# Optimization experiments

Hardware: AMD Instinct MI355X
Metric: run time of the kernel (lower is better)

## Reference

```python
import jax, jax.numpy as jnp
import numpy as np


def setup_inputs() -> dict:
    key = jax.random.key(0)
    k1, k2, k3, k4 = jax.random.split(key, 4)
    NUM_USERS, NUM_ITEMS, EMB_DIM, N_EDGES = 100000, 100000, 64, 1250000
    return {
        "u_emb": 0.1 * jax.random.normal(k1, (NUM_USERS, EMB_DIM), dtype=jnp.float32),
        "i_emb": 0.1 * jax.random.normal(k2, (NUM_ITEMS, EMB_DIM), dtype=jnp.float32),
        "u_idx": jax.random.randint(k3, (N_EDGES,), 0, NUM_USERS, dtype=jnp.int32),
        "i_idx": jax.random.randint(k4, (N_EDGES,), 0, NUM_ITEMS, dtype=jnp.int32),
    }


def reference(u_emb, i_emb, u_idx, i_idx):
    num_users = u_emb.shape[0]
    N = num_users + i_emb.shape[0]
    d = u_emb.shape[1]

    # global item indices; build symmetric directed edge list (2E messages)
    i_g = i_idx + num_users
    src = jnp.concatenate([u_idx, i_g])   # [2E]
    dst = jnp.concatenate([i_g, u_idx])   # [2E]

    # symmetric GCN normalization: w_e = deg(src)^-1/2 * deg(dst)^-1/2
    deg = jnp.zeros((N,), dtype=jnp.float32).at[src].add(1.0)
    d_inv_sqrt = jnp.where(deg > 0, jax.lax.rsqrt(jnp.maximum(deg, 1.0)), 0.0)
    w = d_inv_sqrt[src] * d_inv_sqrt[dst]  # [2E]

    def smooth(x):
        msgs = w[:, None] * x[src]          # [2E, d]
        return jnp.zeros((N, d), dtype=x.dtype).at[dst].add(msgs)

    x0 = jnp.concatenate([u_emb, i_emb], axis=0)  # [N, d]
    x1 = smooth(x0)
    x2 = smooth(x1)
    # embs_list = [x0, x1 + x0, x2 + x1]; mean over the 3 snapshots
    embs = (x0 + (x1 + x0) + (x2 + x1)) / 3.0
    return embs
```

## Files before the change

kernel.cpp:

```cpp
#include <hip/hip_runtime.h>

#define EMB_D 64
#define BN 64
#define LBITS 6
#define SRCBITS 18
#define SRCMASK ((1u << SRCBITS) - 1)
#define CURSTRIDE 16
#define BSCAN_T 256
#define BSCAN_I 16
#define CAPMAX 1280

typedef unsigned short u16;
typedef unsigned int u32;

__device__ __forceinline__ u16 f2bf(float f) {
    u32 u = __float_as_uint(f);
    return (u16)((u + 0x7FFFu + ((u >> 16) & 1u)) >> 16);
}
__device__ __forceinline__ float bf2f(u16 us) {
    return __uint_as_float((u32)us << 16);
}


__global__ void k_hist(const int* __restrict__ u_idx, const int* __restrict__ i_idx,
                       int* __restrict__ counts, int E, int num_users) {
    int e = blockIdx.x * blockDim.x + threadIdx.x;
    if (e < E) {
        int u = __builtin_nontemporal_load(u_idx + e);
        int iv = __builtin_nontemporal_load(i_idx + e);
        atomicAdd(&counts[u], 1);
        atomicAdd(&counts[num_users + iv], 1);
    }
}

__global__ void k_dis(const int* __restrict__ counts, float* __restrict__ dis, int N) {
    int n = blockIdx.x * blockDim.x + threadIdx.x;
    if (n < N) {
        int c = counts[n];
        dis[n] = c > 0 ? rsqrtf((float)c) : 0.0f;
    }
}


__global__ void k_bsize(const int* __restrict__ counts, int* __restrict__ bsize,
                        int N, int nbuckets) {
    int b = blockIdx.x * blockDim.x + threadIdx.x;
    if (b >= nbuckets) return;
    int lo = b << LBITS, hi = min(N, lo + BN);
    int s = 0;
    for (int n = lo; n < hi; n++) s += counts[n];
    bsize[b] = s;
}

__global__ void k_bscan(const int* __restrict__ bsize, int* __restrict__ boff,
                        int* __restrict__ cursors, int nb) {
    __shared__ int ssum[BSCAN_T];
    int t = threadIdx.x;
    int base = t * BSCAN_I;
    int v[BSCAN_I];
    int s = 0;
    for (int k = 0; k < BSCAN_I; k++) {
        int i = base + k;
        v[k] = (i < nb) ? bsize[i] : 0;
        s += v[k];
    }
    ssum[t] = s;
    __syncthreads();
    for (int off = 1; off < BSCAN_T; off <<= 1) {
        int tv = (t >= off) ? ssum[t - off] : 0;
        __syncthreads();
        ssum[t] += tv;
        __syncthreads();
    }
    int run = ssum[t] - s;
    for (int k = 0; k < BSCAN_I; k++) {
        int i = base + k;
        if (i < nb) {
            boff[i] = run;
            cursors[i * CURSTRIDE] = run;
        }
        run += v[k];
    }
    if (t == BSCAN_T - 1) boff[nb] = run;
}

__global__ void k_bucket_fill(const int* __restrict__ u_idx, const int* __restrict__ i_idx,
                              int* __restrict__ cursors, u32* __restrict__ entries,
                              int E, int num_users) {
    int e = blockIdx.x * blockDim.x + threadIdx.x;
    if (e >= E) return;
    int u  = __builtin_nontemporal_load(u_idx + e);
    int ig = num_users + __builtin_nontemporal_load(i_idx + e);
    int p = atomicAdd(&cursors[(u >> LBITS) * CURSTRIDE], 1);
    int q = atomicAdd(&cursors[(ig >> LBITS) * CURSTRIDE], 1);
    entries[p] = ((u32)(u & (BN - 1)) << SRCBITS) | (u32)ig;
    entries[q] = ((u32)(ig & (BN - 1)) << SRCBITS) | (u32)u;
}

__global__ __launch_bounds__(256) void k_bsort(u32* __restrict__ entries,
                                               const int* __restrict__ boff,
                                               int* __restrict__ B, int N) {
    __shared__ u32 se[CAPMAX];
    __shared__ int hcnt[BN];
    __shared__ int hcur[BN];
    int b = blockIdx.x, tid = threadIdx.x;
    int base = boff[b];
    int cnt = boff[b + 1] - base;
    if (cnt > CAPMAX) cnt = CAPMAX;
    for (int i = tid; i < cnt; i += 256) se[i] = entries[base + i];
    if (tid < BN) hcnt[tid] = 0;
    __syncthreads();
    for (int i = tid; i < cnt; i += 256) atomicAdd(&hcnt[se[i] >> SRCBITS], 1);
    __syncthreads();
    if (tid < 64) {
        int v = hcnt[tid];
        int inc = v;
        for (int d = 1; d < 64; d <<= 1) {
            int t = __shfl_up(inc, d);
            if (tid >= d) inc += t;
        }
        int excl = inc - v;
        hcur[tid] = excl;
        int n = (b << LBITS) + tid;
        if (n < N) B[n] = base + excl;
    }
    __syncthreads();
    for (int i = tid; i < cnt; i += 256) {
        u32 e = se[i];
        int dl = (int)(e >> SRCBITS);
        int pos = atomicAdd(&hcur[dl], 1);
        entries[base + pos] = e & SRCMASK;
    }
}

__global__ void k_prescale(const float* __restrict__ ue, const float* __restrict__ ie,
                           const float* __restrict__ dis, u16* __restrict__ xc,
                           int nuD, int totD) {
    int i4 = (blockIdx.x * blockDim.x + threadIdx.x) * 4;
    if (i4 >= totD) return;
    float d = dis[i4 >> 6];
    const float* src = (i4 < nuD) ? (ue + i4) : (ie + (i4 - nuD));
    float4 v = *(const float4*)src;
    u32 p01 = (u32)f2bf(d * v.x) | ((u32)f2bf(d * v.y) << 16);
    u32 p23 = (u32)f2bf(d * v.z) | ((u32)f2bf(d * v.w) << 16);
    *(uint2*)(xc + i4) = make_uint2(p01, p23);
}


__global__ void k_smooth1(const int* __restrict__ B, const int* __restrict__ counts,
                          const u32* __restrict__ adj,
                          const float* __restrict__ dis, const u16* __restrict__ xc0,
                          u16* __restrict__ xc1, int N) {
    int n = blockIdx.x * (blockDim.x >> 6) + (threadIdx.x >> 6);
    int lane = threadIdx.x & 63;
    if (n >= N) return;
    int start = B[n];
    int end = start + counts[n];
    float a0 = 0.f, a1 = 0.f, a2 = 0.f, a3 = 0.f;
    for (int base = start; base < end; base += 64) {
        int cnt = min(64, end - base);
        int nid = 0;
        if (lane < cnt) nid = (int)adj[base + lane];
        int j = 0;
        for (; j + 3 < cnt; j += 4) {
            int n0 = __shfl(nid, j),     n1 = __shfl(nid, j + 1);
            int n2 = __shfl(nid, j + 2), n3 = __shfl(nid, j + 3);
            a0 += bf2f(xc0[((size_t)n0 << 6) + lane]);
            a1 += bf2f(xc0[((size_t)n1 << 6) + lane]);
            a2 += bf2f(xc0[((size_t)n2 << 6) + lane]);
            a3 += bf2f(xc0[((size_t)n3 << 6) + lane]);
        }
        for (; j < cnt; j++) {
            int nj = __shfl(nid, j);
            a0 += bf2f(xc0[((size_t)nj << 6) + lane]);
        }
    }
    float d = dis[n];
    xc1[((size_t)n << 6) + lane] = f2bf(d * d * ((a0 + a1) + (a2 + a3)));
}

__global__ void k_smooth2(const int* __restrict__ B, const int* __restrict__ counts,
                          const u32* __restrict__ adj,
                          const float* __restrict__ dis,
                          const float* __restrict__ u_emb, const float* __restrict__ i_emb,
                          const u16* __restrict__ xc1, float* __restrict__ out,
                          int N, int num_users) {
    int n = blockIdx.x * (blockDim.x >> 6) + (threadIdx.x >> 6);
    int lane = threadIdx.x & 63;
    if (n >= N) return;
    int start = B[n];
    int deg = counts[n];
    int end = start + deg;
    float a0 = 0.f, a1 = 0.f, a2 = 0.f, a3 = 0.f;
    for (int base = start; base < end; base += 64) {
        int cnt = min(64, end - base);
        int nid = 0;
        if (lane < cnt) nid = (int)adj[base + lane];
        int j = 0;
        for (; j + 3 < cnt; j += 4) {
            int n0 = __shfl(nid, j),     n1 = __shfl(nid, j + 1);
            int n2 = __shfl(nid, j + 2), n3 = __shfl(nid, j + 3);
            a0 += bf2f(xc1[((size_t)n0 << 6) + lane]);
            a1 += bf2f(xc1[((size_t)n1 << 6) + lane]);
            a2 += bf2f(xc1[((size_t)n2 << 6) + lane]);
            a3 += bf2f(xc1[((size_t)n3 << 6) + lane]);
        }
        for (; j < cnt; j++) {
            int nj = __shfl(nid, j);
            a0 += bf2f(xc1[((size_t)nj << 6) + lane]);
        }
    }
    size_t o = ((size_t)n << 6) + lane;
    float x0v = (n < num_users) ? u_emb[o] : i_emb[o - (((size_t)num_users) << 6)];
    float x1v = bf2f(xc1[o]) * sqrtf((float)deg);
    out[o] = (2.0f * x0v + 2.0f * x1v + dis[n] * ((a0 + a1) + (a2 + a3))) * (1.0f / 3.0f);
}


extern "C" void kernel_launch(void* const* d_in, const int* in_sizes, int n_in,
                              void* d_out, int out_size, void* d_ws, size_t ws_size,
                              hipStream_t stream) {
    const float* u_emb = (const float*)d_in[0];
    const float* i_emb = (const float*)d_in[1];
    const int*   u_idx = (const int*)d_in[2];
    const int*   i_idx = (const int*)d_in[3];
    float* out = (float*)d_out;

    const int num_users = in_sizes[0] / EMB_D;
    const int num_items = in_sizes[1] / EMB_D;
    const int E = in_sizes[2];
    const int N = num_users + num_items;
    const int adjE = 2 * E;
    const int totD = N * EMB_D;
    const int nuD = num_users * EMB_D;
    const int nbuckets = (N + BN - 1) >> LBITS;

    auto align_up = [](size_t x) { return (x + 255) & ~(size_t)255; };
    char* p = (char*)d_ws;
    int*   counts  = (int*)p; p += align_up((size_t)N * 4);
    float* dis     = (float*)p; p += align_up((size_t)N * 4);
    int*   B       = (int*)p; p += align_up((size_t)N * 4);
    int*   bsize   = (int*)p; p += align_up((size_t)nbuckets * 4);
    int*   boff    = (int*)p; p += align_up((size_t)(nbuckets + 1) * 4);
    int*   cursors = (int*)p; p += align_up((size_t)nbuckets * CURSTRIDE * 4);
    u32*   entries = (u32*)p; p += align_up((size_t)adjE * 4);
    u16*   xc0     = (u16*)p; p += align_up((size_t)totD * 2);
    u16*   xc1     = (u16*)p;

    hipMemsetAsync(counts, 0, (size_t)N * 4, stream);

    const int blk = 256;
    k_hist<<<(E + blk - 1) / blk, blk, 0, stream>>>(u_idx, i_idx, counts, E, num_users);
    k_dis<<<(N + blk - 1) / blk, blk, 0, stream>>>(counts, dis, N);
    k_bsize<<<(nbuckets + blk - 1) / blk, blk, 0, stream>>>(counts, bsize, N, nbuckets);
    k_bscan<<<1, BSCAN_T, 0, stream>>>(bsize, boff, cursors, nbuckets);
    k_bucket_fill<<<(E + blk - 1) / blk, blk, 0, stream>>>(u_idx, i_idx, cursors, entries,
                                                           E, num_users);
    k_bsort<<<nbuckets, blk, 0, stream>>>(entries, boff, B, N);
    k_prescale<<<(totD / 4 + blk - 1) / blk, blk, 0, stream>>>(u_emb, i_emb, dis, xc0,
                                                               nuD, totD);
    int nodes_per_blk = blk / 64;
    int ggrid = (N + nodes_per_blk - 1) / nodes_per_blk;
    k_smooth1<<<ggrid, blk, 0, stream>>>(B, counts, entries, dis, xc0, xc1, N);
    k_smooth2<<<ggrid, blk, 0, stream>>>(B, counts, entries, dis, u_emb, i_emb, xc1, out,
                                         N, num_users);
}
```

Baseline: 542.6 us.

## Partition bucket fill by XCD so each die owns a bucket range

Replaces the per-edge bucket fill with a persistent kernel. Each block reads its XCC_ID and only inserts edges whose destination bucket falls in that die's bucket range. Blocks pull edge chunks from a per-XCD atomic work counter. The aim is to keep cursor atomics and entry writes local to one die's L2 and avoid cross-die coherence traffic, at the cost of every XCD reading the full edge list. Correctness assumes all 8 XCDs get at least one block, since a die with no blocks would leave its buckets unfilled.

```diff
diff --git a/kernel.cpp b/kernel.cpp
--- a/kernel.cpp
+++ b/kernel.cpp
@@ -9,6 +9,8 @@
 #define BSCAN_T 256
 #define BSCAN_I 16
 #define CAPMAX 1280
+#define NXCD 8
+#define CHUNK_IT 8
 
 typedef unsigned short u16;
 typedef unsigned int u32;
@@ -84,17 +86,41 @@
     if (t == BSCAN_T - 1) boff[nb] = run;
 }
 
-__global__ void k_bucket_fill(const int* __restrict__ u_idx, const int* __restrict__ i_idx,
-                              int* __restrict__ cursors, u32* __restrict__ entries,
-                              int E, int num_users) {
-    int e = blockIdx.x * blockDim.x + threadIdx.x;
-    if (e >= E) return;
-    int u  = __builtin_nontemporal_load(u_idx + e);
-    int ig = num_users + __builtin_nontemporal_load(i_idx + e);
-    int p = atomicAdd(&cursors[(u >> LBITS) * CURSTRIDE], 1);
-    int q = atomicAdd(&cursors[(ig >> LBITS) * CURSTRIDE], 1);
-    entries[p] = ((u32)(u & (BN - 1)) << SRCBITS) | (u32)ig;
-    entries[q] = ((u32)(ig & (BN - 1)) << SRCBITS) | (u32)u;
+__global__ void k_fill_xcd(const int* __restrict__ u_idx, const int* __restrict__ i_idx,
+                           int* __restrict__ cursors, u32* __restrict__ entries,
+                           int* __restrict__ chunk_cur, int E, int num_users,
+                           int bucket_range) {
+    u32 xcd;
+    asm("s_getreg_b32 %0, hwreg(HW_REG_XCC_ID)" : "=s"(xcd));
+    xcd &= (NXCD - 1);
+    const int blo = (int)xcd * bucket_range;
+    const int bhi = blo + bucket_range;
+    __shared__ int sbase;
+    const int chunk = 256 * CHUNK_IT;
+    for (;;) {
+        __syncthreads();
+        if (threadIdx.x == 0) sbase = atomicAdd(&chunk_cur[(int)xcd * CURSTRIDE], chunk);
+        __syncthreads();
+        int base = sbase;
+        if (base >= E) break;
+        #pragma unroll
+        for (int k = 0; k < CHUNK_IT; k++) {
+            int e = base + k * 256 + threadIdx.x;
+            if (e < E) {
+                int u  = __builtin_nontemporal_load(u_idx + e);
+                int ig = num_users + __builtin_nontemporal_load(i_idx + e);
+                int bu = u >> LBITS, bi = ig >> LBITS;
+                if (bu >= blo && bu < bhi) {
+                    int p = atomicAdd(&cursors[bu * CURSTRIDE], 1);
+                    entries[p] = ((u32)(u & (BN - 1)) << SRCBITS) | (u32)ig;
+                }
+                if (bi >= blo && bi < bhi) {
+                    int q = atomicAdd(&cursors[bi * CURSTRIDE], 1);
+                    entries[q] = ((u32)(ig & (BN - 1)) << SRCBITS) | (u32)u;
+                }
+            }
+        }
+    }
 }
 
 __global__ __launch_bounds__(256) void k_bsort(u32* __restrict__ entries,
@@ -234,28 +260,31 @@
     const int totD = N * EMB_D;
     const int nuD = num_users * EMB_D;
     const int nbuckets = (N + BN - 1) >> LBITS;
+    const int bucket_range = (nbuckets + NXCD - 1) / NXCD;
 
     auto align_up = [](size_t x) { return (x + 255) & ~(size_t)255; };
     char* p = (char*)d_ws;
-    int*   counts  = (int*)p; p += align_up((size_t)N * 4);
-    float* dis     = (float*)p; p += align_up((size_t)N * 4);
-    int*   B       = (int*)p; p += align_up((size_t)N * 4);
-    int*   bsize   = (int*)p; p += align_up((size_t)nbuckets * 4);
-    int*   boff    = (int*)p; p += align_up((size_t)(nbuckets + 1) * 4);
-    int*   cursors = (int*)p; p += align_up((size_t)nbuckets * CURSTRIDE * 4);
-    u32*   entries = (u32*)p; p += align_up((size_t)adjE * 4);
-    u16*   xc0     = (u16*)p; p += align_up((size_t)totD * 2);
-    u16*   xc1     = (u16*)p;
-
-    hipMemsetAsync(counts, 0, (size_t)N * 4, stream);
+    int*   counts    = (int*)p; p += align_up((size_t)N * 4);
+    int*   chunk_cur = (int*)p; p += align_up((size_t)NXCD * CURSTRIDE * 4);
+    float* dis       = (float*)p; p += align_up((size_t)N * 4);
+    int*   B         = (int*)p; p += align_up((size_t)N * 4);
+    int*   bsize     = (int*)p; p += align_up((size_t)nbuckets * 4);
+    int*   boff      = (int*)p; p += align_up((size_t)(nbuckets + 1) * 4);
+    int*   cursors   = (int*)p; p += align_up((size_t)nbuckets * CURSTRIDE * 4);
+    u32*   entries   = (u32*)p; p += align_up((size_t)adjE * 4);
+    u16*   xc0       = (u16*)p; p += align_up((size_t)totD * 2);
+    u16*   xc1      = (u16*)p;
+
+    hipMemsetAsync(counts, 0, align_up((size_t)N * 4) + align_up((size_t)NXCD * CURSTRIDE * 4),
+                   stream);
 
     const int blk = 256;
     k_hist<<<(E + blk - 1) / blk, blk, 0, stream>>>(u_idx, i_idx, counts, E, num_users);
     k_dis<<<(N + blk - 1) / blk, blk, 0, stream>>>(counts, dis, N);
     k_bsize<<<(nbuckets + blk - 1) / blk, blk, 0, stream>>>(counts, bsize, N, nbuckets);
     k_bscan<<<1, BSCAN_T, 0, stream>>>(bsize, boff, cursors, nbuckets);
-    k_bucket_fill<<<(E + blk - 1) / blk, blk, 0, stream>>>(u_idx, i_idx, cursors, entries,
-                                                           E, num_users);
+    k_fill_xcd<<<512, blk, 0, stream>>>(u_idx, i_idx, cursors, entries, chunk_cur,
+                                        E, num_users, bucket_range);
     k_bsort<<<nbuckets, blk, 0, stream>>>(entries, boff, B, N);
     k_prescale<<<(totD / 4 + blk - 1) / blk, blk, 0, stream>>>(u_emb, i_emb, dis, xc0,
                                                                nuD, totD);
```

After: 540.7 us. No clear change (-0.3%).

## Replace atomic bucket scatter with two-pass LDS-staged radix partition

Applied to the files above, without the earlier changes.

Replaces the per-edge global atomic bucket fill with a two-level radix partition. The first pass groups edges into 4096-node coarse buckets using a shared-memory histogram and one global atomic per bucket per block. The second pass splits each coarse bucket into 64-node buckets the same way. The bsort kernel now stages its sorted output in LDS and writes it back coalesced. The goal is to cut global atomic contention and scattered 4-byte writes, at the cost of an extra recA buffer, an extra full read/write pass over the edges, and more kernel launches.

```diff
diff --git a/kernel.cpp b/kernel.cpp
--- a/kernel.cpp
+++ b/kernel.cpp
@@ -3,12 +3,17 @@
 #define EMB_D 64
 #define BN 64
 #define LBITS 6
+#define CBN 4096
+#define CBBITS 12
 #define SRCBITS 18
 #define SRCMASK ((1u << SRCBITS) - 1)
 #define CURSTRIDE 16
 #define BSCAN_T 256
 #define BSCAN_I 16
 #define CAPMAX 1280
+#define P1_EDGES 1024
+#define P2_RECS 2048
+#define P2_CHUNKS 32
 
 typedef unsigned short u16;
 typedef unsigned int u32;
@@ -84,23 +89,137 @@
     if (t == BSCAN_T - 1) boff[nb] = run;
 }
 
-__global__ void k_bucket_fill(const int* __restrict__ u_idx, const int* __restrict__ i_idx,
-                              int* __restrict__ cursors, u32* __restrict__ entries,
-                              int E, int num_users) {
-    int e = blockIdx.x * blockDim.x + threadIdx.x;
-    if (e >= E) return;
-    int u  = __builtin_nontemporal_load(u_idx + e);
-    int ig = num_users + __builtin_nontemporal_load(i_idx + e);
-    int p = atomicAdd(&cursors[(u >> LBITS) * CURSTRIDE], 1);
-    int q = atomicAdd(&cursors[(ig >> LBITS) * CURSTRIDE], 1);
-    entries[p] = ((u32)(u & (BN - 1)) << SRCBITS) | (u32)ig;
-    entries[q] = ((u32)(ig & (BN - 1)) << SRCBITS) | (u32)u;
+__global__ void k_c1init(const int* __restrict__ boff, int* __restrict__ cursors1,
+                         int nCB, int nbuckets) {
+    int t = threadIdx.x;
+    if (t < nCB) cursors1[t * CURSTRIDE] = boff[min(t * (CBN / BN), nbuckets)];
+}
+
+__global__ __launch_bounds__(256) void k_part1(const int* __restrict__ u_idx,
+                                               const int* __restrict__ i_idx,
+                                               int* __restrict__ cursors1,
+                                               u32* __restrict__ recA,
+                                               int E, int num_users, int nCB) {
+    __shared__ u32 buf[2 * P1_EDGES];
+    __shared__ u16 slotcb[2 * P1_EDGES];
+    __shared__ int hist[64], lofs[64], gbase[64], lcur[64];
+    const int tid = threadIdx.x;
+    const int base = blockIdx.x * P1_EDGES;
+
+    if (tid < 64) hist[tid] = 0;
+    __syncthreads();
+
+    bool val[4]; int ru[4], rig[4];
+    #pragma unroll
+    for (int k = 0; k < 4; k++) {
+        int e = base + k * 256 + tid;
+        val[k] = e < E;
+        ru[k] = 0; rig[k] = 0;
+        if (val[k]) {
+            ru[k]  = __builtin_nontemporal_load(u_idx + e);
+            rig[k] = num_users + __builtin_nontemporal_load(i_idx + e);
+        }
+    }
+    #pragma unroll
+    for (int k = 0; k < 4; k++) if (val[k]) {
+        atomicAdd(&hist[rig[k] >> CBBITS], 1);
+        atomicAdd(&hist[ru[k] >> CBBITS], 1);
+    }
+    __syncthreads();
+    if (tid < 64) {
+        int v = hist[tid], inc = v;
+        for (int d = 1; d < 64; d <<= 1) {
+            int t2 = __shfl_up(inc, d);
+            if ((tid & 63) >= d) inc += t2;
+        }
+        lofs[tid] = inc - v;
+        lcur[tid] = inc - v;
+        gbase[tid] = (tid < nCB) ? atomicAdd(&cursors1[tid * CURSTRIDE], v) : 0;
+    }
+    __syncthreads();
+    #pragma unroll
+    for (int k = 0; k < 4; k++) if (val[k]) {
+        int u = ru[k], ig = rig[k];
+        int cb0 = ig >> CBBITS;
+        int p0 = atomicAdd(&lcur[cb0], 1);
+        buf[p0] = ((u32)(ig & (CBN - 1)) << SRCBITS) | (u32)u;
+        slotcb[p0] = (u16)cb0;
+        int cb1 = u >> CBBITS;
+        int p1 = atomicAdd(&lcur[cb1], 1);
+        buf[p1] = ((u32)(u & (CBN - 1)) << SRCBITS) | (u32)ig;
+        slotcb[p1] = (u16)cb1;
+    }
+    __syncthreads();
+    int tot = 2 * max(0, min(E - base, P1_EDGES));
+    for (int i = tid; i < tot; i += 256) {
+        int cb = slotcb[i];
+        recA[gbase[cb] + (i - lofs[cb])] = buf[i];
+    }
+}
+
+__global__ __launch_bounds__(256) void k_part2(const u32* __restrict__ recA,
+                                               u32* __restrict__ entries,
+                                               int* __restrict__ cursors2,
+                                               const int* __restrict__ boff,
+                                               int nbuckets) {
+    const int b = blockIdx.x / P2_CHUNKS;
+    const int c = blockIdx.x % P2_CHUNKS;
+    const int cbStart = boff[min(b * (CBN / BN), nbuckets)];
+    const int cbEnd   = boff[min((b + 1) * (CBN / BN), nbuckets)];
+    const int start = cbStart + c * P2_RECS;
+    if (start >= cbEnd) return;
+    const int cnt = min(P2_RECS, cbEnd - start);
+
+    __shared__ u32 buf[P2_RECS];
+    __shared__ u16 slotbin[P2_RECS];
+    __shared__ int hist[64], lofs[64], gbase[64], lcur[64];
+    const int tid = threadIdx.x;
+
+    if (tid < 64) hist[tid] = 0;
+    __syncthreads();
+
+    bool rv[8]; u32 rr[8];
+    #pragma unroll
+    for (int k = 0; k < 8; k++) {
+        int i = k * 256 + tid;
+        rv[k] = i < cnt;
+        rr[k] = rv[k] ? recA[start + i] : 0;
+    }
+    #pragma unroll
+    for (int k = 0; k < 8; k++) if (rv[k])
+        atomicAdd(&hist[(rr[k] >> (SRCBITS + LBITS)) & 63], 1);
+    __syncthreads();
+    if (tid < 64) {
+        int v = hist[tid], inc = v;
+        for (int d = 1; d < 64; d <<= 1) {
+            int t2 = __shfl_up(inc, d);
+            if ((tid & 63) >= d) inc += t2;
+        }
+        lofs[tid] = inc - v;
+        lcur[tid] = inc - v;
+        int gb = b * (CBN / BN) + tid;
+        gbase[tid] = (gb < nbuckets) ? atomicAdd(&cursors2[gb * CURSTRIDE], v) : 0;
+    }
+    __syncthreads();
+    #pragma unroll
+    for (int k = 0; k < 8; k++) if (rv[k]) {
+        int bin = (int)((rr[k] >> (SRCBITS + LBITS)) & 63);
+        int pos = atomicAdd(&lcur[bin], 1);
+        buf[pos] = rr[k];
+        slotbin[pos] = (u16)bin;
+    }
+    __syncthreads();
+    for (int i = tid; i < cnt; i += 256) {
+        int bin = slotbin[i];
+        entries[gbase[bin] + (i - lofs[bin])] = buf[i];
+    }
 }
 
 __global__ __launch_bounds__(256) void k_bsort(u32* __restrict__ entries,
                                                const int* __restrict__ boff,
                                                int* __restrict__ B, int N) {
     __shared__ u32 se[CAPMAX];
+    __shared__ u32 se2[CAPMAX];
     __shared__ int hcnt[BN];
     __shared__ int hcur[BN];
     int b = blockIdx.x, tid = threadIdx.x;
@@ -110,7 +229,7 @@
     for (int i = tid; i < cnt; i += 256) se[i] = entries[base + i];
     if (tid < BN) hcnt[tid] = 0;
     __syncthreads();
-    for (int i = tid; i < cnt; i += 256) atomicAdd(&hcnt[se[i] >> SRCBITS], 1);
+    for (int i = tid; i < cnt; i += 256) atomicAdd(&hcnt[(se[i] >> SRCBITS) & 63], 1);
     __syncthreads();
     if (tid < 64) {
         int v = hcnt[tid];
@@ -127,10 +246,12 @@
     __syncthreads();
     for (int i = tid; i < cnt; i += 256) {
         u32 e = se[i];
-        int dl = (int)(e >> SRCBITS);
+        int dl = (int)((e >> SRCBITS) & 63);
         int pos = atomicAdd(&hcur[dl], 1);
-        entries[base + pos] = e & SRCMASK;
-    }
+        se2[pos] = e & SRCMASK;
+    }
+    __syncthreads();
+    for (int i = tid; i < cnt; i += 256) entries[base + i] = se2[i];
 }
 
 __global__ void k_prescale(const float* __restrict__ ue, const float* __restrict__ ie,
@@ -234,18 +355,21 @@
     const int totD = N * EMB_D;
     const int nuD = num_users * EMB_D;
     const int nbuckets = (N + BN - 1) >> LBITS;
+    const int nCB = (N + CBN - 1) >> CBBITS;
 
     auto align_up = [](size_t x) { return (x + 255) & ~(size_t)255; };
     char* p = (char*)d_ws;
-    int*   counts  = (int*)p; p += align_up((size_t)N * 4);
-    float* dis     = (float*)p; p += align_up((size_t)N * 4);
-    int*   B       = (int*)p; p += align_up((size_t)N * 4);
-    int*   bsize   = (int*)p; p += align_up((size_t)nbuckets * 4);
-    int*   boff    = (int*)p; p += align_up((size_t)(nbuckets + 1) * 4);
-    int*   cursors = (int*)p; p += align_up((size_t)nbuckets * CURSTRIDE * 4);
-    u32*   entries = (u32*)p; p += align_up((size_t)adjE * 4);
-    u16*   xc0     = (u16*)p; p += align_up((size_t)totD * 2);
-    u16*   xc1     = (u16*)p;
+    int*   counts   = (int*)p; p += align_up((size_t)N * 4);
+    float* dis      = (float*)p; p += align_up((size_t)N * 4);
+    int*   B        = (int*)p; p += align_up((size_t)N * 4);
+    int*   bsize    = (int*)p; p += align_up((size_t)nbuckets * 4);
+    int*   boff     = (int*)p; p += align_up((size_t)(nbuckets + 1) * 4);
+    int*   cursors2 = (int*)p; p += align_up((size_t)nbuckets * CURSTRIDE * 4);
+    int*   cursors1 = (int*)p; p += align_up((size_t)64 * CURSTRIDE * 4);
+    u32*   recA     = (u32*)p; p += align_up((size_t)adjE * 4);
+    u32*   entries  = (u32*)p; p += align_up((size_t)adjE * 4);
+    u16*   xc0      = (u16*)p; p += align_up((size_t)totD * 2);
+    u16*   xc1      = (u16*)p;
 
     hipMemsetAsync(counts, 0, (size_t)N * 4, stream);
 
@@ -253,9 +377,11 @@
     k_hist<<<(E + blk - 1) / blk, blk, 0, stream>>>(u_idx, i_idx, counts, E, num_users);
     k_dis<<<(N + blk - 1) / blk, blk, 0, stream>>>(counts, dis, N);
     k_bsize<<<(nbuckets + blk - 1) / blk, blk, 0, stream>>>(counts, bsize, N, nbuckets);
-    k_bscan<<<1, BSCAN_T, 0, stream>>>(bsize, boff, cursors, nbuckets);
-    k_bucket_fill<<<(E + blk - 1) / blk, blk, 0, stream>>>(u_idx, i_idx, cursors, entries,
-                                                           E, num_users);
+    k_bscan<<<1, BSCAN_T, 0, stream>>>(bsize, boff, cursors2, nbuckets);
+    k_c1init<<<1, 64, 0, stream>>>(boff, cursors1, nCB, nbuckets);
+    k_part1<<<(E + P1_EDGES - 1) / P1_EDGES, blk, 0, stream>>>(
+        u_idx, i_idx, cursors1, recA, E, num_users, nCB);
+    k_part2<<<nCB * P2_CHUNKS, blk, 0, stream>>>(recA, entries, cursors2, boff, nbuckets);
     k_bsort<<<nbuckets, blk, 0, stream>>>(entries, boff, B, N);
     k_prescale<<<(totD / 4 + blk - 1) / blk, blk, 0, stream>>>(u_emb, i_emb, dis, xc0,
                                                                nuD, totD);
```

Measured after the change: 460.1 us. 15.2% less time.
